# Performance work log

Hardware: AMD Instinct MI355X
Metric: run time of the kernel (lower is better)

## Reference

```python
import jax, jax.numpy as jnp
import numpy as np

N_NODES = 100000
M_EDGES = 500000
D = 128
L = 2
LRELU_SLOPE = 0.01
LN_EPS = 1e-5


def layer_norm(x, g, b):
    mu = jnp.mean(x, axis=-1, keepdims=True)
    var = jnp.var(x, axis=-1, keepdims=True)
    return (x - mu) * jax.lax.rsqrt(var + LN_EPS) * g + b


def leaky_relu(x):
    return jnp.where(x >= 0, x, LRELU_SLOPE * x)


def setup_inputs() -> dict:
    key = jax.random.key(0)
    ks = jax.random.split(key, 12)
    s = 1.0 / np.sqrt(D)
    inp = {
        "H": jax.random.normal(ks[0], (N_NODES, D), jnp.float32),
        "E": jax.random.normal(ks[1], (M_EDGES, D), jnp.float32),
        "ht": jax.random.randint(ks[2], (M_EDGES, 2), 0, N_NODES, jnp.int64) if jax.config.jax_enable_x64 else jax.random.randint(ks[2], (M_EDGES, 2), 0, N_NODES).astype(jnp.int32),
        "queries": jax.random.randint(ks[3], (M_EDGES,), 0, 2).astype(jnp.int32),
        # per-layer params stacked on leading L axis
        "W_eu": jax.random.uniform(ks[4], (L, 3 * D, D), jnp.float32, -s, s),
        "b_eu": jnp.zeros((L, D), jnp.float32),
        "ln_e_g": jnp.ones((L, D), jnp.float32),
        "ln_e_b": jnp.zeros((L, D), jnp.float32),
        "W_fwd": jax.random.uniform(ks[5], (L, 2 * D, D), jnp.float32, -s, s),
        "b_fwd": jnp.zeros((L, D), jnp.float32),
        "W_back": jax.random.uniform(ks[6], (L, 2 * D, D), jnp.float32, -s, s),
        "b_back": jnp.zeros((L, D), jnp.float32),
        "ln_h_g": jnp.ones((L, D), jnp.float32),
        "ln_h_b": jnp.zeros((L, D), jnp.float32),
    }
    return inp


def aggregate_messages(ht, messages_fwd, messages_back, n):
    # destinations: fwd msgs go to tails, back msgs go to heads
    msg_dst = jnp.concatenate([ht[:, 1], ht[:, 0]])  # [2m]
    messages = jnp.concatenate([messages_fwd, messages_back], axis=0)  # [2m, d]
    agg = jax.ops.segment_sum(messages, msg_dst, num_segments=n)  # [n, d]
    counts = jax.ops.segment_sum(jnp.ones_like(msg_dst, jnp.float32), msg_dst, num_segments=n)
    # torch yields nan/inf for count-0 nodes; clamp to 1 (0/1 = 0) for stability
    return agg / jnp.maximum(counts, 1.0)[:, None]


def reference(H, E, ht, queries, W_eu, b_eu, ln_e_g, ln_e_b,
              W_fwd, b_fwd, W_back, b_back, ln_h_g, ln_h_b):
    n = H.shape[0]
    for l in range(L):
        # --- EdgeUpdateLayer ---
        head_rep = H[ht[:, 0]]  # [m, d]
        tail_rep = H[ht[:, 1]]  # [m, d]
        triple = jnp.concatenate([head_rep, E, tail_rep], axis=1)  # [m, 3d]
        eu = leaky_relu(triple @ W_eu[l] + b_eu[l])
        E = layer_norm(eu + E, ln_e_g[l], ln_e_b[l])
        # --- MessagePassingLayer ---
        msgs_fwd = jnp.concatenate([H[ht[:, 0]], E], axis=1) @ W_fwd[l] + b_fwd[l]
        msgs_back = jnp.concatenate([H[ht[:, 1]], E], axis=1) @ W_back[l] + b_back[l]
        agg = aggregate_messages(ht, msgs_fwd, msgs_back, n)
        H = layer_norm(leaky_relu(agg) + H, ln_h_g[l], ln_h_b[l])
    return H
```

## Files before the change

kernel.cpp:

```cpp
#include <hip/hip_runtime.h>

#define N_NODES 100000
#define M_EDGES 500000
#define D 128
#define SLOPE 0.01f
#define EPS 1e-5f

typedef __attribute__((ext_vector_type(8))) short bf16x8;
typedef __attribute__((ext_vector_type(4))) float f32x4;
typedef __attribute__((ext_vector_type(4))) unsigned int u32x4;

__device__ __forceinline__ unsigned short f2bf(float f) {
    union { float f; unsigned u; } v; v.f = f;
    unsigned r = v.u + 0x7FFF + ((v.u >> 16) & 1);
    return (unsigned short)(r >> 16);
}
__device__ __forceinline__ float bf2f(unsigned short u) {
    union { unsigned u; float f; } v; v.u = ((unsigned)u) << 16; return v.f;
}
__device__ __forceinline__ u32x4 pack8v(f32x4 a, f32x4 b) {
    u32x4 r;
    r.x = ((unsigned)f2bf(a.y) << 16) | f2bf(a.x);
    r.y = ((unsigned)f2bf(a.w) << 16) | f2bf(a.z);
    r.z = ((unsigned)f2bf(b.y) << 16) | f2bf(b.x);
    r.w = ((unsigned)f2bf(b.w) << 16) | f2bf(b.z);
    return r;
}
#define GXT(v, nt) bf2f((unsigned short)(((nt) & 1) ? ((v)[(nt) >> 1] >> 16) : ((v)[(nt) >> 1] & 0xffff)))

__global__ void wconv_kernel(const float* __restrict__ src, unsigned short* __restrict__ dst,
                             int K, int total)
{
    int i = blockIdx.x * 256 + threadIdx.x;
    if (i >= total) return;
    int layer_sz = K * 128;
    int l = i / layer_sz;
    int r = i - l * layer_sz;
    int j    = r & 7;
    int lane = (r >> 3) & 63;
    int nt   = (r >> 9) & 7;
    int kk   = r >> 12;
    int row  = kk * 32 + ((lane >> 4) << 3) + j;
    int col  = nt * 16 + (lane & 15);
    dst[i] = f2bf(src[(size_t)l * layer_sz + row * 128 + col]);
}

__global__ void h2b_kernel(const float* __restrict__ src, unsigned short* __restrict__ dst, int total8)
{
    int i = blockIdx.x * 256 + threadIdx.x;
    if (i >= total8) return;
    f32x4 a = ((const f32x4*)src)[2 * i];
    f32x4 b = ((const f32x4*)src)[2 * i + 1];
    ((u32x4*)dst)[i] = pack8v(a, b);
}

__global__ void count_kernel(const int* __restrict__ ht, int* __restrict__ cnt, int m)
{
    int e = blockIdx.x * 256 + threadIdx.x;
    if (e < m) {
        atomicAdd(&cnt[ht[2 * e]],     1);
        atomicAdd(&cnt[ht[2 * e + 1]], 1);
    }
}

__global__ void scanA_kernel(const int* __restrict__ cnt, int* __restrict__ partial,
                             int* __restrict__ bsum, int n)
{
    __shared__ int tmp[256];
    int t = threadIdx.x, i = blockIdx.x * 256 + t;
    int v = (i < n) ? cnt[i] : 0;
    tmp[t] = v;
    __syncthreads();
    for (int s = 1; s < 256; s <<= 1) {
        int x = (t >= s) ? tmp[t - s] : 0;
        __syncthreads();
        tmp[t] += x;
        __syncthreads();
    }
    if (i < n) partial[i] = tmp[t] - v;
    if (t == 255) bsum[blockIdx.x] = tmp[255];
}

__global__ void scanB_kernel(int* __restrict__ bsum, int nb)
{
    __shared__ int tmp[512];
    int t = threadIdx.x;
    int v = (t < nb) ? bsum[t] : 0;
    tmp[t] = v;
    __syncthreads();
    for (int s = 1; s < 512; s <<= 1) {
        int x = (t >= s) ? tmp[t - s] : 0;
        __syncthreads();
        tmp[t] += x;
        __syncthreads();
    }
    if (t < nb) bsum[t] = tmp[t] - v;
}

__global__ void scanC_kernel(const int* __restrict__ partial, const int* __restrict__ bsum,
                             int* __restrict__ off, int* __restrict__ pos, int n)
{
    int i = blockIdx.x * 256 + threadIdx.x;
    if (i < n) {
        int o = partial[i] + bsum[blockIdx.x];
        off[i] = o;
        pos[i] = o;
    }
    if (i == 0) off[n] = 2 * M_EDGES;
}

__global__ void fill_kernel(const int* __restrict__ ht, int* __restrict__ pos,
                            int* __restrict__ slotF, int* __restrict__ slotB, int m)
{
    int e = blockIdx.x * 256 + threadIdx.x;
    if (e < m) {
        int2 p = ((const int2*)ht)[e];
        slotF[e] = atomicAdd(&pos[p.y], 1);
        slotB[e] = atomicAdd(&pos[p.x], 1);
    }
}

__global__ __launch_bounds__(256, 2)
void hw_kernel(const unsigned short* __restrict__ Hb,
               const unsigned short* __restrict__ B0,
               const unsigned short* __restrict__ B1,
               const unsigned short* __restrict__ B2,
               const unsigned short* __restrict__ B3,
               unsigned short* __restrict__ HW)
{
    __shared__ unsigned short bsh[16384];

    const int tid = threadIdx.x;
    const int wv  = tid >> 6;
    const int ln  = tid & 63;
    const int g   = ln >> 4;
    const int c15 = ln & 15;
    const int mb  = blockIdx.x >> 2;
    const int grp = blockIdx.x & 3;

    const unsigned short* Bsel = (grp == 0) ? B0 : (grp == 1) ? B1 : (grp == 2) ? B2 : B3;

    {
        const u32x4* bs = (const u32x4*)Bsel;
        u32x4* bd = (u32x4*)bsh;
#pragma unroll
        for (int it = 0; it < 8; ++it) bd[it * 256 + tid] = bs[it * 256 + tid];
    }

    const int rb = mb * 128 + wv * 32;
    const unsigned short* arow[2];
#pragma unroll
    for (int m = 0; m < 2; ++m) {
        int r = rb + m * 16 + c15;
        if (r >= N_NODES) r = N_NODES - 1;
        arow[m] = Hb + (size_t)r * 128;
    }
    __syncthreads();

    f32x4 acc[2][8];
#pragma unroll
    for (int m = 0; m < 2; ++m)
#pragma unroll
        for (int nt = 0; nt < 8; ++nt) acc[m][nt] = (f32x4){0.f, 0.f, 0.f, 0.f};

#pragma unroll
    for (int kk = 0; kk < 4; ++kk) {
        bf16x8 a[2];
#pragma unroll
        for (int m = 0; m < 2; ++m) a[m] = *(const bf16x8*)(arow[m] + kk * 32 + g * 8);
#pragma unroll
        for (int nt = 0; nt < 8; ++nt) {
            bf16x8 b = *(const bf16x8*)(bsh + (kk * 8 + nt) * 512 + ln * 8);
#pragma unroll
            for (int m = 0; m < 2; ++m)
                acc[m][nt] = __builtin_amdgcn_mfma_f32_16x16x32_bf16(a[m], b, acc[m][nt], 0, 0, 0);
        }
    }

#pragma unroll
    for (int m = 0; m < 2; ++m) {
#pragma unroll
        for (int rr = 0; rr < 4; ++rr) {
            int rg = rb + m * 16 + g * 4 + rr;
            if (rg < N_NODES) {
                u32x4 o;
                o.x = ((unsigned)f2bf(acc[m][1][rr]) << 16) | f2bf(acc[m][0][rr]);
                o.y = ((unsigned)f2bf(acc[m][3][rr]) << 16) | f2bf(acc[m][2][rr]);
                o.z = ((unsigned)f2bf(acc[m][5][rr]) << 16) | f2bf(acc[m][4][rr]);
                o.w = ((unsigned)f2bf(acc[m][7][rr]) << 16) | f2bf(acc[m][6][rr]);
                *(u32x4*)(HW + (size_t)rg * 512 + grp * 128 + c15 * 8) = o;
            }
        }
    }
}

template <bool E_F32, bool WRITE_E>
__global__ __launch_bounds__(64, 2)
void edge_mfma_kernel(const unsigned short* __restrict__ HW,
                      const float* __restrict__ E0,
                      const unsigned short* __restrict__ Ebf,
                      unsigned short* __restrict__ Eout,
                      const int* __restrict__ ht,
                      const unsigned short* __restrict__ Weu,
                      const unsigned short* __restrict__ Wf,
                      const unsigned short* __restrict__ Wb,
                      const float* __restrict__ beu,
                      const float* __restrict__ lneg, const float* __restrict__ lneb,
                      const float* __restrict__ bfw, const float* __restrict__ bbw,
                      const int* __restrict__ slotF, const int* __restrict__ slotB,
                      unsigned short* __restrict__ msg)
{
    __shared__ unsigned char en[8192];

    const int ln  = threadIdx.x;
    const int g   = ln >> 4;
    const int c15 = ln & 15;
    const int ew0 = blockIdx.x * 32;

    const int slotFv = slotF[ew0 + (ln & 31)];
    const int slotBv = slotB[ew0 + (ln & 31)];

    int hid[2][4], tln[2][4];
#pragma unroll
    for (int m = 0; m < 2; ++m)
#pragma unroll
        for (int rr = 0; rr < 4; ++rr) {
            int2 p = ((const int2*)ht)[ew0 + m * 16 + g * 4 + rr];
            hid[m][rr] = p.x;
            tln[m][rr] = p.y;
        }

    u32x4 ga[2][4], gc[2][4];
#pragma unroll
    for (int m = 0; m < 2; ++m)
#pragma unroll
        for (int rr = 0; rr < 4; ++rr) {
            ga[m][rr] = *(const u32x4*)(HW + (size_t)hid[m][rr] * 512 + c15 * 8);
            gc[m][rr] = *(const u32x4*)(HW + (size_t)tln[m][rr] * 512 + 128 + c15 * 8);
        }

#pragma unroll
    for (int it = 0; it < 8; ++it) {
        int lin = it * 1024 + ln * 16;
        int row = lin >> 8;
        int e   = ew0 + row;
        int elem = (lin & 255) >> 1;
        u32x4 pk;
        if (E_F32) {
            const float* s = E0 + (size_t)e * D + elem;
            pk = pack8v(*(const f32x4*)s, *(const f32x4*)(s + 4));
        } else {
            pk = *(const u32x4*)(Ebf + (size_t)e * D + elem);
        }
        *(u32x4*)(en + (lin ^ ((row & 7) << 4))) = pk;
    }

    const int ebase0 = c15 * 256 + g * 16;
    const int ebase1 = (16 + c15) * 256 + g * 16;
    const int swz    = (c15 & 7) << 4;

    f32x4 acc[2][8];

#pragma unroll
    for (int m = 0; m < 2; ++m)
#pragma unroll
        for (int nt = 0; nt < 8; ++nt) acc[m][nt] = (f32x4){0.f, 0.f, 0.f, 0.f};
    {
        const u32x4* Wg = (const u32x4*)Weu;
        u32x4 bc[8];
        bf16x8 a0, a1, a0n, a1n;
#pragma unroll
        for (int nt = 0; nt < 8; ++nt) bc[nt] = Wg[4 * 512 + nt * 64 + ln];
        a0 = *(const bf16x8*)(en + (ebase0 ^ swz));
        a1 = *(const bf16x8*)(en + (ebase1 ^ swz));
#pragma unroll
        for (int kk = 0; kk < 4; ++kk) {
            if (kk < 3) {
                a0n = *(const bf16x8*)(en + ((ebase0 + (kk + 1) * 64) ^ swz));
                a1n = *(const bf16x8*)(en + ((ebase1 + (kk + 1) * 64) ^ swz));
            }
#pragma unroll
            for (int nt = 0; nt < 8; ++nt) {
                bf16x8 b = *(const bf16x8*)&bc[nt];
                acc[0][nt] = __builtin_amdgcn_mfma_f32_16x16x32_bf16(a0, b, acc[0][nt], 0, 0, 0);
                acc[1][nt] = __builtin_amdgcn_mfma_f32_16x16x32_bf16(a1, b, acc[1][nt], 0, 0, 0);
                if (kk < 3) bc[nt] = Wg[(5 + kk) * 512 + nt * 64 + ln];
            }
            a0 = a0n; a1 = a1n;
        }
    }

    {
        float be[8], lg[8], lb[8];
#pragma unroll
        for (int nt = 0; nt < 8; ++nt) {
            be[nt] = beu[nt * 16 + c15];
            lg[nt] = lneg[nt * 16 + c15];
            lb[nt] = lneb[nt * 16 + c15];
        }
#pragma unroll
        for (int m = 0; m < 2; ++m) {
            float s[4] = {0.f,0.f,0.f,0.f}, ss[4] = {0.f,0.f,0.f,0.f};
#pragma unroll
            for (int nt = 0; nt < 8; ++nt) {
#pragma unroll
                for (int r = 0; r < 4; ++r) {
                    int row = m * 16 + g * 4 + r;
                    float x = acc[m][nt][r] + GXT(ga[m][r], nt) + GXT(gc[m][r], nt) + be[nt];
                    x = (x >= 0.f) ? x : SLOPE * x;
                    int lin = row * 256 + (nt * 16 + c15) * 2;
                    x += bf2f(*(const unsigned short*)(en + (lin ^ ((row & 7) << 4))));
                    acc[m][nt][r] = x;
                    s[r] += x; ss[r] += x * x;
                }
            }
#pragma unroll
            for (int d = 1; d < 16; d <<= 1) {
#pragma unroll
                for (int r = 0; r < 4; ++r) {
                    s[r]  += __shfl_xor(s[r],  d);
                    ss[r] += __shfl_xor(ss[r], d);
                }
            }
            float mu[4], rs[4];
#pragma unroll
            for (int r = 0; r < 4; ++r) {
                mu[r] = s[r] * (1.0f / 128.0f);
                float var = ss[r] * (1.0f / 128.0f) - mu[r] * mu[r];
                rs[r] = rsqrtf(var + EPS);
            }
#pragma unroll
            for (int nt = 0; nt < 8; ++nt) {
#pragma unroll
                for (int r = 0; r < 4; ++r) {
                    int row = m * 16 + g * 4 + r;
                    float xn = (acc[m][nt][r] - mu[r]) * rs[r] * lg[nt] + lb[nt];
                    int lin = row * 256 + (nt * 16 + c15) * 2;
                    *(unsigned short*)(en + (lin ^ ((row & 7) << 4))) = f2bf(xn);
                }
            }
        }
    }

    if (WRITE_E) {
#pragma unroll
        for (int it = 0; it < 8; ++it) {
            int lin = it * 1024 + ln * 16;
            int row = lin >> 8;
            *(u32x4*)(Eout + (size_t)(ew0 + row) * D + ((lin & 255) >> 1)) =
                *(const u32x4*)(en + (lin ^ ((row & 7) << 4)));
        }
    }

#pragma unroll 1
    for (int p = 0; p < 2; ++p) {
        const u32x4* Wg = (const u32x4*)(p ? Wb : Wf);
        const float* bias = p ? bbw : bfw;
        const int slotv = p ? slotBv : slotFv;

        u32x4 gm[2][4];
#pragma unroll
        for (int m = 0; m < 2; ++m)
#pragma unroll
            for (int rr = 0; rr < 4; ++rr) {
                int node = p ? tln[m][rr] : hid[m][rr];
                gm[m][rr] = *(const u32x4*)(HW + (size_t)node * 512 + 256 + p * 128 + c15 * 8);
            }

#pragma unroll
        for (int m = 0; m < 2; ++m)
#pragma unroll
            for (int nt = 0; nt < 8; ++nt) acc[m][nt] = (f32x4){0.f, 0.f, 0.f, 0.f};
        {
            u32x4 bc[8];
            bf16x8 a0, a1, a0n, a1n;
#pragma unroll
            for (int nt = 0; nt < 8; ++nt) bc[nt] = Wg[4 * 512 + nt * 64 + ln];
            a0 = *(const bf16x8*)(en + (ebase0 ^ swz));
            a1 = *(const bf16x8*)(en + (ebase1 ^ swz));
#pragma unroll
            for (int kk = 0; kk < 4; ++kk) {
                if (kk < 3) {
                    a0n = *(const bf16x8*)(en + ((ebase0 + (kk + 1) * 64) ^ swz));
                    a1n = *(const bf16x8*)(en + ((ebase1 + (kk + 1) * 64) ^ swz));
                }
#pragma unroll
                for (int nt = 0; nt < 8; ++nt) {
                    bf16x8 b = *(const bf16x8*)&bc[nt];
                    acc[0][nt] = __builtin_amdgcn_mfma_f32_16x16x32_bf16(a0, b, acc[0][nt], 0, 0, 0);
                    acc[1][nt] = __builtin_amdgcn_mfma_f32_16x16x32_bf16(a1, b, acc[1][nt], 0, 0, 0);
                    if (kk < 3) bc[nt] = Wg[(5 + kk) * 512 + nt * 64 + ln];
                }
                a0 = a0n; a1 = a1n;
            }
        }

        {
            float bv[8];
#pragma unroll
            for (int nt = 0; nt < 8; ++nt) bv[nt] = bias[nt * 16 + c15];
#pragma unroll
            for (int m = 0; m < 2; ++m) {
#pragma unroll
                for (int r = 0; r < 4; ++r) {
                    int erow = m * 16 + g * 4 + r;
                    int slot = __shfl(slotv, erow);
                    unsigned* base = (unsigned*)(msg + (size_t)slot * D + (c15 & ~1));
#pragma unroll
                    for (int nt = 0; nt < 8; ++nt) {
                        float v = acc[m][nt][r] + GXT(gm[m][r], nt) + bv[nt];
                        float o = __shfl_xor(v, 1);
                        float lo = (ln & 1) ? o : v;
                        float hi = (ln & 1) ? v : o;
                        unsigned pk = ((unsigned)f2bf(hi) << 16) | f2bf(lo);
                        if ((ln & 1) == (nt >> 2))
                            base[nt * 8] = pk;
                    }
                }
            }
        }
    }
}

__global__ __launch_bounds__(256)
void node_kernel(const float* __restrict__ Hin, const unsigned short* __restrict__ msg,
                 const int* __restrict__ off, const float* __restrict__ g,
                 const float* __restrict__ b, float* __restrict__ Hout,
                 unsigned short* __restrict__ Hb, int n)
{
    const int wave = threadIdx.x >> 6, lane = threadIdx.x & 63;
    const int node = blockIdx.x * 4 + wave;
    if (node >= n) return;

    const int beg = off[node], end = off[node + 1];
    const float inv = 1.0f / fmaxf((float)(end - beg), 1.0f);
    const unsigned* mb = (const unsigned*)msg;

    float a0 = 0.f, a1 = 0.f;
    int i = beg;
    for (; i + 1 < end; i += 2) {
        unsigned v0 = mb[(size_t)i * 64 + lane];
        unsigned v1 = mb[(size_t)(i + 1) * 64 + lane];
        a0 += bf2f((unsigned short)(v0 & 0xffff)) + bf2f((unsigned short)(v1 & 0xffff));
        a1 += bf2f((unsigned short)(v0 >> 16))    + bf2f((unsigned short)(v1 >> 16));
    }
    if (i < end) {
        unsigned v0 = mb[(size_t)i * 64 + lane];
        a0 += bf2f((unsigned short)(v0 & 0xffff));
        a1 += bf2f((unsigned short)(v0 >> 16));
    }

    a0 *= inv; a1 *= inv;
    a0 = (a0 >= 0.f) ? a0 : SLOPE * a0;
    a1 = (a1 >= 0.f) ? a1 : SLOPE * a1;

    size_t base = (size_t)node * D + 2 * lane;
    float x0 = a0 + Hin[base];
    float x1 = a1 + Hin[base + 1];

    float s = x0 + x1, ss = x0 * x0 + x1 * x1;
#pragma unroll
    for (int d = 1; d < 64; d <<= 1) {
        s  += __shfl_xor(s, d);
        ss += __shfl_xor(ss, d);
    }
    float mu  = s * (1.0f / 128.0f);
    float var = ss * (1.0f / 128.0f) - mu * mu;
    float rs  = rsqrtf(var + EPS);

    float o0 = (x0 - mu) * rs * g[2 * lane]     + b[2 * lane];
    float o1 = (x1 - mu) * rs * g[2 * lane + 1] + b[2 * lane + 1];
    Hout[base]     = o0;
    Hout[base + 1] = o1;
    Hb[base]       = f2bf(o0);
    Hb[base + 1]   = f2bf(o1);
}

extern "C" void kernel_launch(void* const* d_in, const int* in_sizes, int n_in,
                              void* d_out, int out_size, void* d_ws, size_t ws_size,
                              hipStream_t stream)
{
    const float* H0   = (const float*)d_in[0];
    const float* E0   = (const float*)d_in[1];
    const int*   ht   = (const int*)d_in[2];
    const float* Weu  = (const float*)d_in[4];
    const float* beu  = (const float*)d_in[5];
    const float* lneg = (const float*)d_in[6];
    const float* lneb = (const float*)d_in[7];
    const float* Wf   = (const float*)d_in[8];
    const float* bfw  = (const float*)d_in[9];
    const float* Wb   = (const float*)d_in[10];
    const float* bbw  = (const float*)d_in[11];
    const float* lnhg = (const float*)d_in[12];
    const float* lnhb = (const float*)d_in[13];

    float* Hout = (float*)d_out;

    char* ws = (char*)d_ws;
    unsigned short* msg    = (unsigned short*)(ws);
    unsigned short* Ebuf   = (unsigned short*)(ws + 256000000);
    unsigned short* HW     = (unsigned short*)(ws + 384000000);
    unsigned short* Hb     = (unsigned short*)(ws + 486400000);
    unsigned short* Weu_sw = (unsigned short*)(ws + 512000000);
    unsigned short* Wf_sw  = (unsigned short*)(ws + 512196608);
    unsigned short* Wb_sw  = (unsigned short*)(ws + 512327680);
    int*            cnt    = (int*)(ws + 512458752);
    int*            partial= (int*)(ws + 512858752);
    int*            bsum   = (int*)(ws + 513258752);
    int*            off    = (int*)(ws + 513260800);
    int*            pos    = (int*)(ws + 513660816);
    int*            slotF  = (int*)(ws + 514060816);
    int*            slotB  = (int*)(ws + 516060816);

    wconv_kernel<<<(2*384*128 + 255)/256, 256, 0, stream>>>(Weu, Weu_sw, 384, 2*384*128);
    wconv_kernel<<<(2*256*128 + 255)/256, 256, 0, stream>>>(Wf,  Wf_sw,  256, 2*256*128);
    wconv_kernel<<<(2*256*128 + 255)/256, 256, 0, stream>>>(Wb,  Wb_sw,  256, 2*256*128);
    h2b_kernel<<<(N_NODES * D / 8 + 255)/256, 256, 0, stream>>>(H0, Hb, N_NODES * D / 8);

    const int nscan = (N_NODES + 255) / 256;
    hipMemsetAsync(cnt, 0, (size_t)N_NODES * sizeof(int), stream);
    count_kernel<<<(M_EDGES + 255) / 256, 256, 0, stream>>>(ht, cnt, M_EDGES);
    scanA_kernel<<<nscan, 256, 0, stream>>>(cnt, partial, bsum, N_NODES);
    scanB_kernel<<<1, 512, 0, stream>>>(bsum, nscan);
    scanC_kernel<<<nscan, 256, 0, stream>>>(partial, bsum, off, pos, N_NODES);
    fill_kernel<<<(M_EDGES + 255) / 256, 256, 0, stream>>>(ht, pos, slotF, slotB, M_EDGES);

    const int hwblocks = ((N_NODES + 127) / 128) * 4;
    const int eblocks  = M_EDGES / 32;

    for (int l = 0; l < 2; ++l) {
        const float* Hin = (l == 0) ? H0 : Hout;
        const unsigned short* WeuL = Weu_sw + (size_t)l * 49152;
        const unsigned short* WfL  = Wf_sw  + (size_t)l * 32768;
        const unsigned short* WbL  = Wb_sw  + (size_t)l * 32768;

        hw_kernel<<<hwblocks, 256, 0, stream>>>(
            Hb, WeuL, WeuL + 8 * 4096, WfL, WbL, HW);

        if (l == 0) {
            edge_mfma_kernel<true, true><<<eblocks, 64, 0, stream>>>(
                HW, E0, nullptr, Ebuf, ht, WeuL, WfL, WbL,
                beu, lneg, lneb, bfw, bbw, slotF, slotB, msg);
        } else {
            edge_mfma_kernel<false, false><<<eblocks, 64, 0, stream>>>(
                HW, nullptr, Ebuf, nullptr, ht, WeuL, WfL, WbL,
                beu + D, lneg + D, lneb + D, bfw + D, bbw + D, slotF, slotB, msg);
        }

        node_kernel<<<(N_NODES + 3) / 4, 256, 0, stream>>>(
            Hin, msg, off, lnhg + (size_t)l * D, lnhb + (size_t)l * D, Hout, Hb, N_NODES);
    }
}
```

Baseline: 863.1 us.

## Make edge kernel persistent with register-prefetched next tile of E

Turns the edge MFMA kernel into a persistent grid of 2048 single-wave blocks that loop over 32-edge tiles, prefetching the next tile's E rows and slot indices into registers while the current tile computes. The fp32-to-bf16 conversion of E moves into a separate pre-pass kernel, so the edge kernel always reads bf16 and updates E in place. This aims to hide global-load latency. In exchange it uses more registers, adds a full extra pass over E, and the smaller grid may reduce occupancy and latency hiding.

```diff
diff --git a/kernel.cpp b/kernel.cpp
--- a/kernel.cpp
+++ b/kernel.cpp
@@ -5,6 +5,8 @@
 #define D 128
 #define SLOPE 0.01f
 #define EPS 1e-5f
+#define NTILES 15625
+#define EGRID 2048
 
 typedef __attribute__((ext_vector_type(8))) short bf16x8;
 typedef __attribute__((ext_vector_type(4))) float f32x4;
@@ -194,12 +196,10 @@
     }
 }
 
-template <bool E_F32, bool WRITE_E>
+template <bool WRITE_E>
 __global__ __launch_bounds__(64, 2)
 void edge_mfma_kernel(const unsigned short* __restrict__ HW,
-                      const float* __restrict__ E0,
-                      const unsigned short* __restrict__ Ebf,
-                      unsigned short* __restrict__ Eout,
+                      unsigned short* __restrict__ Ebf,
                       const int* __restrict__ ht,
                       const unsigned short* __restrict__ Weu,
                       const unsigned short* __restrict__ Wf,
@@ -215,163 +215,77 @@
     const int ln  = threadIdx.x;
     const int g   = ln >> 4;
     const int c15 = ln & 15;
-    const int ew0 = blockIdx.x * 32;
-
-    const int slotFv = slotF[ew0 + (ln & 31)];
-    const int slotBv = slotB[ew0 + (ln & 31)];
-
-    int hid[2][4], tln[2][4];
-#pragma unroll
-    for (int m = 0; m < 2; ++m)
-#pragma unroll
-        for (int rr = 0; rr < 4; ++rr) {
-            int2 p = ((const int2*)ht)[ew0 + m * 16 + g * 4 + rr];
-            hid[m][rr] = p.x;
-            tln[m][rr] = p.y;
-        }
-
-    u32x4 ga[2][4], gc[2][4];
-#pragma unroll
-    for (int m = 0; m < 2; ++m)
-#pragma unroll
-        for (int rr = 0; rr < 4; ++rr) {
-            ga[m][rr] = *(const u32x4*)(HW + (size_t)hid[m][rr] * 512 + c15 * 8);
-            gc[m][rr] = *(const u32x4*)(HW + (size_t)tln[m][rr] * 512 + 128 + c15 * 8);
-        }
-
-#pragma unroll
-    for (int it = 0; it < 8; ++it) {
-        int lin = it * 1024 + ln * 16;
-        int row = lin >> 8;
-        int e   = ew0 + row;
-        int elem = (lin & 255) >> 1;
-        u32x4 pk;
-        if (E_F32) {
-            const float* s = E0 + (size_t)e * D + elem;
-            pk = pack8v(*(const f32x4*)s, *(const f32x4*)(s + 4));
-        } else {
-            pk = *(const u32x4*)(Ebf + (size_t)e * D + elem);
-        }
-        *(u32x4*)(en + (lin ^ ((row & 7) << 4))) = pk;
-    }
-
     const int ebase0 = c15 * 256 + g * 16;
     const int ebase1 = (16 + c15) * 256 + g * 16;
     const int swz    = (c15 & 7) << 4;
 
-    f32x4 acc[2][8];
-
-#pragma unroll
-    for (int m = 0; m < 2; ++m)
-#pragma unroll
-        for (int nt = 0; nt < 8; ++nt) acc[m][nt] = (f32x4){0.f, 0.f, 0.f, 0.f};
+    u32x4 sreg[8];
+    int sF, sB;
+
+    int tile = blockIdx.x;
     {
-        const u32x4* Wg = (const u32x4*)Weu;
-        u32x4 bc[8];
-        bf16x8 a0, a1, a0n, a1n;
-#pragma unroll
-        for (int nt = 0; nt < 8; ++nt) bc[nt] = Wg[4 * 512 + nt * 64 + ln];
-        a0 = *(const bf16x8*)(en + (ebase0 ^ swz));
-        a1 = *(const bf16x8*)(en + (ebase1 ^ swz));
-#pragma unroll
-        for (int kk = 0; kk < 4; ++kk) {
-            if (kk < 3) {
-                a0n = *(const bf16x8*)(en + ((ebase0 + (kk + 1) * 64) ^ swz));
-                a1n = *(const bf16x8*)(en + ((ebase1 + (kk + 1) * 64) ^ swz));
-            }
-#pragma unroll
-            for (int nt = 0; nt < 8; ++nt) {
-                bf16x8 b = *(const bf16x8*)&bc[nt];
-                acc[0][nt] = __builtin_amdgcn_mfma_f32_16x16x32_bf16(a0, b, acc[0][nt], 0, 0, 0);
-                acc[1][nt] = __builtin_amdgcn_mfma_f32_16x16x32_bf16(a1, b, acc[1][nt], 0, 0, 0);
-                if (kk < 3) bc[nt] = Wg[(5 + kk) * 512 + nt * 64 + ln];
-            }
-            a0 = a0n; a1 = a1n;
-        }
-    }
-
-    {
-        float be[8], lg[8], lb[8];
-#pragma unroll
-        for (int nt = 0; nt < 8; ++nt) {
-            be[nt] = beu[nt * 16 + c15];
-            lg[nt] = lneg[nt * 16 + c15];
-            lb[nt] = lneb[nt * 16 + c15];
-        }
-#pragma unroll
-        for (int m = 0; m < 2; ++m) {
-            float s[4] = {0.f,0.f,0.f,0.f}, ss[4] = {0.f,0.f,0.f,0.f};
-#pragma unroll
-            for (int nt = 0; nt < 8; ++nt) {
-#pragma unroll
-                for (int r = 0; r < 4; ++r) {
-                    int row = m * 16 + g * 4 + r;
-                    float x = acc[m][nt][r] + GXT(ga[m][r], nt) + GXT(gc[m][r], nt) + be[nt];
-                    x = (x >= 0.f) ? x : SLOPE * x;
-                    int lin = row * 256 + (nt * 16 + c15) * 2;
-                    x += bf2f(*(const unsigned short*)(en + (lin ^ ((row & 7) << 4))));
-                    acc[m][nt][r] = x;
-                    s[r] += x; ss[r] += x * x;
-                }
-            }
-#pragma unroll
-            for (int d = 1; d < 16; d <<= 1) {
-#pragma unroll
-                for (int r = 0; r < 4; ++r) {
-                    s[r]  += __shfl_xor(s[r],  d);
-                    ss[r] += __shfl_xor(ss[r], d);
-                }
-            }
-            float mu[4], rs[4];
-#pragma unroll
-            for (int r = 0; r < 4; ++r) {
-                mu[r] = s[r] * (1.0f / 128.0f);
-                float var = ss[r] * (1.0f / 128.0f) - mu[r] * mu[r];
-                rs[r] = rsqrtf(var + EPS);
-            }
-#pragma unroll
-            for (int nt = 0; nt < 8; ++nt) {
-#pragma unroll
-                for (int r = 0; r < 4; ++r) {
-                    int row = m * 16 + g * 4 + r;
-                    float xn = (acc[m][nt][r] - mu[r]) * rs[r] * lg[nt] + lb[nt];
-                    int lin = row * 256 + (nt * 16 + c15) * 2;
-                    *(unsigned short*)(en + (lin ^ ((row & 7) << 4))) = f2bf(xn);
-                }
-            }
-        }
-    }
-
-    if (WRITE_E) {
+        int base = tile * 32;
 #pragma unroll
         for (int it = 0; it < 8; ++it) {
             int lin = it * 1024 + ln * 16;
             int row = lin >> 8;
-            *(u32x4*)(Eout + (size_t)(ew0 + row) * D + ((lin & 255) >> 1)) =
-                *(const u32x4*)(en + (lin ^ ((row & 7) << 4)));
-        }
+            sreg[it] = *(const u32x4*)(Ebf + (size_t)(base + row) * D + ((lin & 255) >> 1));
+        }
+        sF = slotF[base + (ln & 31)];
+        sB = slotB[base + (ln & 31)];
     }
 
 #pragma unroll 1
-    for (int p = 0; p < 2; ++p) {
-        const u32x4* Wg = (const u32x4*)(p ? Wb : Wf);
-        const float* bias = p ? bbw : bfw;
-        const int slotv = p ? slotBv : slotFv;
-
-        u32x4 gm[2][4];
+    for (; tile < NTILES; tile += EGRID) {
+        const int ew0 = tile * 32;
+
+#pragma unroll
+        for (int it = 0; it < 8; ++it) {
+            int lin = it * 1024 + ln * 16;
+            int row = lin >> 8;
+            *(u32x4*)(en + (lin ^ ((row & 7) << 4))) = sreg[it];
+        }
+        const int slotFv = sF, slotBv = sB;
+
+        int hid[2][4], tid_[2][4];
 #pragma unroll
         for (int m = 0; m < 2; ++m)
 #pragma unroll
             for (int rr = 0; rr < 4; ++rr) {
-                int node = p ? tln[m][rr] : hid[m][rr];
-                gm[m][rr] = *(const u32x4*)(HW + (size_t)node * 512 + 256 + p * 128 + c15 * 8);
-            }
+                int2 p = ((const int2*)ht)[ew0 + m * 16 + g * 4 + rr];
+                hid[m][rr] = p.x;
+                tid_[m][rr] = p.y;
+            }
+        u32x4 ga[2][4], gc[2][4];
+#pragma unroll
+        for (int m = 0; m < 2; ++m)
+#pragma unroll
+            for (int rr = 0; rr < 4; ++rr) {
+                ga[m][rr] = *(const u32x4*)(HW + (size_t)hid[m][rr] * 512 + c15 * 8);
+                gc[m][rr] = *(const u32x4*)(HW + (size_t)tid_[m][rr] * 512 + 128 + c15 * 8);
+            }
+
+        {
+            int nt0 = tile + EGRID; if (nt0 >= NTILES) nt0 = tile;
+            int base = nt0 * 32;
+#pragma unroll
+            for (int it = 0; it < 8; ++it) {
+                int lin = it * 1024 + ln * 16;
+                int row = lin >> 8;
+                sreg[it] = *(const u32x4*)(Ebf + (size_t)(base + row) * D + ((lin & 255) >> 1));
+            }
+            sF = slotF[base + (ln & 31)];
+            sB = slotB[base + (ln & 31)];
+        }
+
+        f32x4 acc[2][8];
 
 #pragma unroll
         for (int m = 0; m < 2; ++m)
 #pragma unroll
             for (int nt = 0; nt < 8; ++nt) acc[m][nt] = (f32x4){0.f, 0.f, 0.f, 0.f};
         {
+            const u32x4* Wg = (const u32x4*)Weu;
             u32x4 bc[8];
             bf16x8 a0, a1, a0n, a1n;
 #pragma unroll
@@ -396,25 +310,131 @@
         }
 
         {
-            float bv[8];
-#pragma unroll
-            for (int nt = 0; nt < 8; ++nt) bv[nt] = bias[nt * 16 + c15];
+            float be[8], lg[8], lb[8];
+#pragma unroll
+            for (int nt = 0; nt < 8; ++nt) {
+                be[nt] = beu[nt * 16 + c15];
+                lg[nt] = lneg[nt * 16 + c15];
+                lb[nt] = lneb[nt * 16 + c15];
+            }
 #pragma unroll
             for (int m = 0; m < 2; ++m) {
+                float s[4] = {0.f,0.f,0.f,0.f}, ss[4] = {0.f,0.f,0.f,0.f};
+#pragma unroll
+                for (int nt = 0; nt < 8; ++nt) {
+#pragma unroll
+                    for (int r = 0; r < 4; ++r) {
+                        int row = m * 16 + g * 4 + r;
+                        float x = acc[m][nt][r] + GXT(ga[m][r], nt) + GXT(gc[m][r], nt) + be[nt];
+                        x = (x >= 0.f) ? x : SLOPE * x;
+                        int lin = row * 256 + (nt * 16 + c15) * 2;
+                        x += bf2f(*(const unsigned short*)(en + (lin ^ ((row & 7) << 4))));
+                        acc[m][nt][r] = x;
+                        s[r] += x; ss[r] += x * x;
+                    }
+                }
+#pragma unroll
+                for (int d = 1; d < 16; d <<= 1) {
+#pragma unroll
+                    for (int r = 0; r < 4; ++r) {
+                        s[r]  += __shfl_xor(s[r],  d);
+                        ss[r] += __shfl_xor(ss[r], d);
+                    }
+                }
+                float mu[4], rs[4];
 #pragma unroll
                 for (int r = 0; r < 4; ++r) {
-                    int erow = m * 16 + g * 4 + r;
-                    int slot = __shfl(slotv, erow);
-                    unsigned* base = (unsigned*)(msg + (size_t)slot * D + (c15 & ~1));
+                    mu[r] = s[r] * (1.0f / 128.0f);
+                    float var = ss[r] * (1.0f / 128.0f) - mu[r] * mu[r];
+                    rs[r] = rsqrtf(var + EPS);
+                }
+#pragma unroll
+                for (int nt = 0; nt < 8; ++nt) {
+#pragma unroll
+                    for (int r = 0; r < 4; ++r) {
+                        int row = m * 16 + g * 4 + r;
+                        float xn = (acc[m][nt][r] - mu[r]) * rs[r] * lg[nt] + lb[nt];
+                        int lin = row * 256 + (nt * 16 + c15) * 2;
+                        *(unsigned short*)(en + (lin ^ ((row & 7) << 4))) = f2bf(xn);
+                    }
+                }
+            }
+        }
+
+        if (WRITE_E) {
+#pragma unroll
+            for (int it = 0; it < 8; ++it) {
+                int lin = it * 1024 + ln * 16;
+                int row = lin >> 8;
+                *(u32x4*)(Ebf + (size_t)(ew0 + row) * D + ((lin & 255) >> 1)) =
+                    *(const u32x4*)(en + (lin ^ ((row & 7) << 4)));
+            }
+        }
+
+#pragma unroll 1
+        for (int p = 0; p < 2; ++p) {
+            const u32x4* Wg = (const u32x4*)(p ? Wb : Wf);
+            const float* bias = p ? bbw : bfw;
+            const int slotv = p ? slotBv : slotFv;
+
+            u32x4 gm[2][4];
+#pragma unroll
+            for (int m = 0; m < 2; ++m)
+#pragma unroll
+                for (int rr = 0; rr < 4; ++rr) {
+                    int node = p ? tid_[m][rr] : hid[m][rr];
+                    gm[m][rr] = *(const u32x4*)(HW + (size_t)node * 512 + 256 + p * 128 + c15 * 8);
+                }
+
+#pragma unroll
+            for (int m = 0; m < 2; ++m)
+#pragma unroll
+                for (int nt = 0; nt < 8; ++nt) acc[m][nt] = (f32x4){0.f, 0.f, 0.f, 0.f};
+            {
+                u32x4 bc[8];
+                bf16x8 a0, a1, a0n, a1n;
+#pragma unroll
+                for (int nt = 0; nt < 8; ++nt) bc[nt] = Wg[4 * 512 + nt * 64 + ln];
+                a0 = *(const bf16x8*)(en + (ebase0 ^ swz));
+                a1 = *(const bf16x8*)(en + (ebase1 ^ swz));
+#pragma unroll
+                for (int kk = 0; kk < 4; ++kk) {
+                    if (kk < 3) {
+                        a0n = *(const bf16x8*)(en + ((ebase0 + (kk + 1) * 64) ^ swz));
+                        a1n = *(const bf16x8*)(en + ((ebase1 + (kk + 1) * 64) ^ swz));
+                    }
 #pragma unroll
                     for (int nt = 0; nt < 8; ++nt) {
-                        float v = acc[m][nt][r] + GXT(gm[m][r], nt) + bv[nt];
-                        float o = __shfl_xor(v, 1);
-                        float lo = (ln & 1) ? o : v;
-                        float hi = (ln & 1) ? v : o;
-                        unsigned pk = ((unsigned)f2bf(hi) << 16) | f2bf(lo);
-                        if ((ln & 1) == (nt >> 2))
-                            base[nt * 8] = pk;
+                        bf16x8 b = *(const bf16x8*)&bc[nt];
+                        acc[0][nt] = __builtin_amdgcn_mfma_f32_16x16x32_bf16(a0, b, acc[0][nt], 0, 0, 0);
+                        acc[1][nt] = __builtin_amdgcn_mfma_f32_16x16x32_bf16(a1, b, acc[1][nt], 0, 0, 0);
+                        if (kk < 3) bc[nt] = Wg[(5 + kk) * 512 + nt * 64 + ln];
+                    }
+                    a0 = a0n; a1 = a1n;
+                }
+            }
+
+            {
+                float bv[8];
+#pragma unroll
+                for (int nt = 0; nt < 8; ++nt) bv[nt] = bias[nt * 16 + c15];
+#pragma unroll
+                for (int m = 0; m < 2; ++m) {
+#pragma unroll
+                    for (int r = 0; r < 4; ++r) {
+                        int erow = m * 16 + g * 4 + r;
+                        int slot = __shfl(slotv, erow);
+                        unsigned* base = (unsigned*)(msg + (size_t)slot * D + (c15 & ~1));
+#pragma unroll
+                        for (int nt = 0; nt < 8; ++nt) {
+                            float v = acc[m][nt][r] + GXT(gm[m][r], nt) + bv[nt];
+                            float o = __shfl_xor(v, 1);
+                            float lo = (ln & 1) ? o : v;
+                            float hi = (ln & 1) ? v : o;
+                            unsigned pk = ((unsigned)f2bf(hi) << 16) | f2bf(lo);
+                            if ((ln & 1) == (nt >> 2))
+                                base[nt * 8] = pk;
+                        }
                     }
                 }
             }
@@ -516,6 +536,7 @@
     wconv_kernel<<<(2*256*128 + 255)/256, 256, 0, stream>>>(Wf,  Wf_sw,  256, 2*256*128);
     wconv_kernel<<<(2*256*128 + 255)/256, 256, 0, stream>>>(Wb,  Wb_sw,  256, 2*256*128);
     h2b_kernel<<<(N_NODES * D / 8 + 255)/256, 256, 0, stream>>>(H0, Hb, N_NODES * D / 8);
+    h2b_kernel<<<(M_EDGES * D / 8 + 255)/256, 256, 0, stream>>>(E0, Ebuf, M_EDGES * D / 8);
 
     const int nscan = (N_NODES + 255) / 256;
     hipMemsetAsync(cnt, 0, (size_t)N_NODES * sizeof(int), stream);
@@ -526,7 +547,6 @@
     fill_kernel<<<(M_EDGES + 255) / 256, 256, 0, stream>>>(ht, pos, slotF, slotB, M_EDGES);
 
     const int hwblocks = ((N_NODES + 127) / 128) * 4;
-    const int eblocks  = M_EDGES / 32;
 
     for (int l = 0; l < 2; ++l) {
         const float* Hin = (l == 0) ? H0 : Hout;
@@ -538,12 +558,12 @@
             Hb, WeuL, WeuL + 8 * 4096, WfL, WbL, HW);
 
         if (l == 0) {
-            edge_mfma_kernel<true, true><<<eblocks, 64, 0, stream>>>(
-                HW, E0, nullptr, Ebuf, ht, WeuL, WfL, WbL,
+            edge_mfma_kernel<true><<<EGRID, 64, 0, stream>>>(
+                HW, Ebuf, ht, WeuL, WfL, WbL,
                 beu, lneg, lneb, bfw, bbw, slotF, slotB, msg);
         } else {
-            edge_mfma_kernel<false, false><<<eblocks, 64, 0, stream>>>(
-                HW, nullptr, Ebuf, nullptr, ht, WeuL, WfL, WbL,
+            edge_mfma_kernel<false><<<EGRID, 64, 0, stream>>>(
+                HW, Ebuf, ht, WeuL, WfL, WbL,
                 beu + D, lneg + D, lneb + D, bfw + D, bbw + D, slotF, slotB, msg);
         }
 
```

New measurement: 1.317 ms. 52.6% more time.
